# Kernel tuning notes

Measured on AMD Instinct MI355X. Metric: run time of the kernel, lower is better.

The kernel has to match this reference:

```python
import jax, jax.numpy as jnp
import numpy as np

N, E, G = 50000, 800000, 512
IN_C, H, EC, L, OUT_C = 16, 128, 16, 4, 1

def _lin(k, fi, fo):
    return jax.random.normal(k, (fi, fo), dtype=jnp.float32) / np.sqrt(fi)

def setup_inputs() -> dict:
    key = jax.random.key(0)
    ks = jax.random.split(key, 32)
    inp = {
        'x_nodes': jax.random.normal(ks[0], (N, IN_C), dtype=jnp.float32),
        'x_edges': jax.random.normal(ks[1], (E, EC), dtype=jnp.float32),
        'edge_index': jax.random.randint(ks[2], (2, E), 0, N),
        'batch': jnp.sort(jax.random.randint(ks[3], (N,), 0, G)),
    }
    # embed_nodes
    inp['emb_w1'] = _lin(ks[4], IN_C, H); inp['emb_b1'] = jnp.zeros((H,), jnp.float32)
    inp['emb_w2'] = _lin(ks[5], H, H);    inp['emb_b2'] = jnp.zeros((H,), jnp.float32)
    # per-layer edge_net / node_net weights, stacked over L
    kk = jax.random.split(ks[6], 4 * L)
    inp['ew1'] = jnp.stack([_lin(kk[i], 2 * H + EC, H) for i in range(L)])
    inp['eb1'] = jnp.zeros((L, H), jnp.float32)
    inp['ew2'] = jnp.stack([_lin(kk[L + i], H, H) for i in range(L)])
    inp['eb2'] = jnp.zeros((L, H), jnp.float32)
    inp['nw1'] = jnp.stack([_lin(kk[2 * L + i], 2 * H, H) for i in range(L)])
    inp['nb1'] = jnp.zeros((L, H), jnp.float32)
    inp['nw2'] = jnp.stack([_lin(kk[3 * L + i], H, H) for i in range(L)])
    inp['nb2'] = jnp.zeros((L, H), jnp.float32)
    # pre_readout / readout
    inp['pr_w1'] = _lin(ks[7], H, H); inp['pr_b1'] = jnp.zeros((H,), jnp.float32)
    inp['pr_w2'] = _lin(ks[8], H, H); inp['pr_b2'] = jnp.zeros((H,), jnp.float32)
    inp['ro_w1'] = _lin(ks[9], H, H); inp['ro_b1'] = jnp.zeros((H,), jnp.float32)
    inp['ro_w2'] = _lin(ks[10], H, OUT_C); inp['ro_b2'] = jnp.zeros((OUT_C,), jnp.float32)
    return inp

def _gnn_forward(x_nodes, x_edges, emb_w1, emb_b1, emb_w2, emb_b2,
                 ew1, eb1, ew2, eb2, nw1, nb1, nw2, nb2,
                 pr_w1, pr_b1, pr_w2, pr_b2, ro_w1, ro_b1, ro_w2, ro_b2,
                 edge_index, batch):
    silu = jax.nn.silu
    sender, receiver = edge_index[0], edge_index[1]
    # embed_nodes
    h = silu(x_nodes @ emb_w1 + emb_b1) @ emb_w2 + emb_b2  # [N, H]
    for l in range(L):
        state = jnp.concatenate((h[sender], h[receiver], x_edges), axis=1)  # [E, 2H+EC]
        msg = silu(silu(state @ ew1[l] + eb1[l]) @ ew2[l] + eb2[l])  # [E, H]
        aggr = jax.ops.segment_sum(msg, receiver, num_segments=N)  # [N, H]
        h = silu(jnp.concatenate((h, aggr), axis=1) @ nw1[l] + nb1[l]) @ nw2[l] + nb2[l]
    h = silu(h @ pr_w1 + pr_b1) @ pr_w2 + pr_b2
    pooled = jax.ops.segment_sum(h, batch, num_segments=G)  # [G, H]
    out = silu(pooled @ ro_w1 + ro_b1) @ ro_w2 + ro_b2  # [G, 1]
    return jnp.squeeze(out)

def reference(x_nodes, x_edges, edge_index, batch,
              emb_w1, emb_b1, emb_w2, emb_b2,
              ew1, eb1, ew2, eb2, nw1, nb1, nw2, nb2,
              pr_w1, pr_b1, pr_w2, pr_b2, ro_w1, ro_b1, ro_w2, ro_b2):
    return _gnn_forward(x_nodes, x_edges, emb_w1, emb_b1, emb_w2, emb_b2,
                        ew1, eb1, ew2, eb2, nw1, nb1, nw2, nb2,
                        pr_w1, pr_b1, pr_w2, pr_b2, ro_w1, ro_b1, ro_w2, ro_b2,
                        edge_index, batch)
```

## Files before the change

### kernel.cpp

```cpp
#include <hip/hip_runtime.h>


typedef short bf16x8 __attribute__((ext_vector_type(8)));
typedef float f32x4 __attribute__((ext_vector_type(4)));

union U8 { bf16x8 v; unsigned short u[8]; unsigned int d[4]; };

__device__ __forceinline__ float bf2f(unsigned short u) {
    union { unsigned int i; float f; } x; x.i = ((unsigned int)u) << 16; return x.f;
}
__device__ __forceinline__ float u32lo2f(unsigned int d) {
    union { unsigned int i; float f; } x; x.i = d << 16; return x.f;
}
__device__ __forceinline__ float u32hi2f(unsigned int d) {
    union { unsigned int i; float f; } x; x.i = d & 0xffff0000u; return x.f;
}
__device__ __forceinline__ unsigned short f2bf(float f) {
    union { float f; unsigned int i; } x; x.f = f;
    unsigned int r = x.i + 0x7FFFu + ((x.i >> 16) & 1u);
    return (unsigned short)(r >> 16);
}
__device__ __forceinline__ unsigned int cvt_pk_bf16(float lo, float hi) {
    unsigned int r;
    asm("v_cvt_pk_bf16_f32 %0, %1, %2" : "=v"(r) : "v"(lo), "v"(hi));
    return r;
}
__device__ __forceinline__ float siluf(float x) { return x / (1.0f + __expf(-x)); }
__device__ __forceinline__ float silu_fast(float x) {
    float e;
    asm("v_exp_f32 %0, %1" : "=v"(e) : "v"(x * -1.44269504089f));
    float r;
    asm("v_rcp_f32 %0, %1" : "=v"(r) : "v"(e + 1.0f));
    return x * r;
}

__global__ void k_hist(const int* __restrict__ recv, int* __restrict__ counts, int E) {
    int i = blockIdx.x * 256 + threadIdx.x;
    if (i < E) atomicAdd(&counts[recv[i]], 1);
}

__global__ __launch_bounds__(1024) void k_scan1(const int* __restrict__ counts,
                                                int* __restrict__ offsets,
                                                int* __restrict__ bsum, int n) {
    __shared__ int buf[1024];
    int i = blockIdx.x * 1024 + threadIdx.x;
    int v = (i < n) ? counts[i] : 0;
    buf[threadIdx.x] = v;
    __syncthreads();
    for (int off = 1; off < 1024; off <<= 1) {
        int t = 0;
        if ((int)threadIdx.x >= off) t = buf[threadIdx.x - off];
        __syncthreads();
        if ((int)threadIdx.x >= off) buf[threadIdx.x] += t;
        __syncthreads();
    }
    if (i < n) offsets[i] = buf[threadIdx.x] - v;
    if (threadIdx.x == 1023) bsum[blockIdx.x] = buf[1023];
}

__global__ void k_scan2(int* __restrict__ bsum, int nb) {
    if (threadIdx.x == 0 && blockIdx.x == 0) {
        int acc = 0;
        for (int b = 0; b < nb; ++b) { int v = bsum[b]; bsum[b] = acc; acc += v; }
    }
}

__global__ __launch_bounds__(1024) void k_scan3(int* __restrict__ offsets,
                                                const int* __restrict__ bsum,
                                                int n, int E) {
    int i = blockIdx.x * 1024 + threadIdx.x;
    if (i < n) offsets[i] += bsum[blockIdx.x];
    if (i == 0) offsets[n] = E;
}

__global__ void k_scatter(const int* __restrict__ send, const int* __restrict__ recv,
                          const int* __restrict__ offsets, int* __restrict__ cursor,
                          int* __restrict__ ss, int* __restrict__ sr,
                          int* __restrict__ perm, int E) {
    int i = blockIdx.x * 256 + threadIdx.x;
    if (i < E) {
        int r = recv[i];
        int pos = offsets[r] + atomicAdd(&cursor[r], 1);
        ss[pos] = send[i];
        sr[pos] = r;
        perm[pos] = i;
    }
}

__global__ void k_permute_xe(const float* __restrict__ xe, const int* __restrict__ perm,
                             unsigned short* __restrict__ out, int E) {
    int t = blockIdx.x * 256 + threadIdx.x;
    if (t < E * 4) {
        int pos = t >> 2, q = t & 3;
        int e = perm[pos];
        float4 v = *(const float4*)(xe + (size_t)e * 16 + q * 4);
        ushort4 o;
        o.x = f2bf(v.x); o.y = f2bf(v.y); o.z = f2bf(v.z); o.w = f2bf(v.w);
        *(ushort4*)(out + (size_t)pos * 16 + q * 4) = o;
    }
}

struct WJob { const float* src; unsigned short* dst; int rows; int perm; };
struct WJobs { WJob j[31]; };

__global__ __launch_bounds__(256) void k_wconv(WJobs jobs) {
    WJob jb = jobs.j[blockIdx.x];
    int n = jb.rows * 128;
    if (jb.perm) {
        for (int i = threadIdx.x; i < n; i += 256) {
            int c = i >> 7, slot = i & 127;
            int feat = (slot >> 3) + 16 * (slot & 7);
            jb.dst[c * 128 + slot] = f2bf(jb.src[feat * 128 + c]);
        }
    } else {
        for (int i = threadIdx.x; i < n; i += 256) {
            int k = i >> 7, c = i & 127;
            jb.dst[c * jb.rows + k] = f2bf(jb.src[i]);
        }
    }
}

__global__ __launch_bounds__(256) void k_embed1(const float* __restrict__ x,
                                                const float* __restrict__ w1,
                                                const float* __restrict__ b1,
                                                unsigned short* __restrict__ out, int N) {
    int idx = blockIdx.x * 256 + threadIdx.x;
    int n = idx >> 6, lane = idx & 63;
    if (n >= N) return;
    const float* xr = x + (size_t)n * 16;
    float xv[16];
#pragma unroll
    for (int k = 0; k < 16; k += 4) {
        float4 v = *(const float4*)(xr + k);
        xv[k] = v.x; xv[k + 1] = v.y; xv[k + 2] = v.z; xv[k + 3] = v.w;
    }
    int c0 = lane * 2;
    float a0 = b1[c0], a1 = b1[c0 + 1];
#pragma unroll
    for (int k = 0; k < 16; ++k) {
        float2 w = *(const float2*)(w1 + k * 128 + c0);
        a0 += xv[k] * w.x; a1 += xv[k] * w.y;
    }
    *(unsigned int*)(out + (size_t)n * 128 + c0) = cvt_pk_bf16(siluf(a0), siluf(a1));
}

__device__ __forceinline__ void load_frags(const unsigned short* __restrict__ A,
                                           int r0, int colb, int kg, int M,
                                           bf16x8 (&Af)[2][4]) {
#pragma unroll
    for (int rf = 0; rf < 2; ++rf) {
        int row = r0 + rf * 16 + colb;
        if (row < M) {
#pragma unroll
            for (int ks = 0; ks < 4; ++ks)
                Af[rf][ks] = *(const bf16x8*)(A + (size_t)row * 128 + ks * 32 + kg * 8);
        } else {
            U8 z;
#pragma unroll
            for (int i = 0; i < 8; ++i) z.u[i] = 0;
#pragma unroll
            for (int ks = 0; ks < 4; ++ks) Af[rf][ks] = z.v;
        }
    }
}

__device__ __forceinline__ void mma_block(const bf16x8 (&Af)[2][4],
                                          const unsigned short* sW,
                                          int colb, int kg, f32x4 (&C)[2][8]) {
#pragma unroll
    for (int ks = 0; ks < 4; ++ks) {
#pragma unroll
        for (int cf = 0; cf < 8; ++cf) {
            bf16x8 B = *(const bf16x8*)(sW + (colb + 16 * cf) * 136 + ks * 32 + kg * 8);
#pragma unroll
            for (int rf = 0; rf < 2; ++rf)
                C[rf][cf] = __builtin_amdgcn_mfma_f32_16x16x32_bf16(Af[rf][ks], B, C[rf][cf], 0, 0, 0);
        }
    }
}

#define WLOAD(WT) do { \
    _Pragma("unroll") \
    for (int k_ = 0; k_ < 8; ++k_) \
        wreg[k_] = *(const bf16x8*)((WT) + tid * 8 + k_ * 2048); \
} while (0)

#define WWRITE() do { __syncthreads(); \
    _Pragma("unroll") \
    for (int k_ = 0; k_ < 8; ++k_) { \
        int i_ = tid * 8 + k_ * 2048; \
        *(bf16x8*)(sW + (i_ >> 7) * 136 + (i_ & 127)) = wreg[k_]; \
    } \
    __syncthreads(); } while (0)

__global__ __launch_bounds__(256, 2) void k_node(
    const unsigned short* __restrict__ A1, const unsigned short* __restrict__ WT1,
    const unsigned short* __restrict__ A2, const unsigned short* __restrict__ WT2,
    const float* __restrict__ b12, int act1,
    unsigned short* __restrict__ out1,
    const unsigned short* __restrict__ WT3, const float* __restrict__ b3,
    unsigned short* __restrict__ out3,
    const unsigned short* __restrict__ WTs, const unsigned short* __restrict__ WTr,
    unsigned short* __restrict__ outPs, unsigned short* __restrict__ outPr,
    int M) {
    __shared__ unsigned short sW[128 * 136];
    __shared__ unsigned short sT[128 * 136];
    int tid = threadIdx.x, lane = tid & 63, w = tid >> 6;
    int r0 = blockIdx.x * 128 + w * 32;
    int colb = lane & 15, kg = lane >> 4;
    bf16x8 wreg[8];

    f32x4 C[2][8];
#pragma unroll
    for (int cf = 0; cf < 8; ++cf) {
        float bb = b12[colb + 16 * cf];
        C[0][cf] = (f32x4){bb, bb, bb, bb};
        C[1][cf] = C[0][cf];
    }
    bf16x8 Af[2][4], Af2[2][4];
    WLOAD(WT1);
    load_frags(A1, r0, colb, kg, M, Af);
    if (WT2) load_frags(A2, r0, colb, kg, M, Af2);
    WWRITE();
    if (WT2) WLOAD(WT2);
    mma_block(Af, sW, colb, kg, C);
    if (WT2) {
        WWRITE();
        if (WT3) WLOAD(WT3);
        mma_block(Af2, sW, colb, kg, C);
    } else if (WT3) {
        WLOAD(WT3);
    }
#pragma unroll
    for (int rf = 0; rf < 2; ++rf) {
#pragma unroll
        for (int cf = 0; cf < 8; ++cf) {
            int col = colb + 16 * cf;
#pragma unroll
            for (int j = 0; j < 4; ++j) {
                float v = C[rf][cf][j];
                if (act1) v = siluf(v);
                unsigned short bv = f2bf(v);
                int lrow = w * 32 + rf * 16 + kg * 4 + j;
                sT[lrow * 136 + col] = bv;
                if (out1) {
                    int row = r0 + rf * 16 + kg * 4 + j;
                    if (row < M) out1[(size_t)row * 128 + col] = bv;
                }
            }
        }
    }

    if (WT3) {
        WWRITE();
        if (WTs) WLOAD(WTs);
        bf16x8 At[2][4];
#pragma unroll
        for (int rf = 0; rf < 2; ++rf)
#pragma unroll
            for (int ks = 0; ks < 4; ++ks)
                At[rf][ks] = *(const bf16x8*)(sT + (w * 32 + rf * 16 + colb) * 136 + ks * 32 + kg * 8);
#pragma unroll
        for (int cf = 0; cf < 8; ++cf) {
            float bb = b3[colb + 16 * cf];
            C[0][cf] = (f32x4){bb, bb, bb, bb};
            C[1][cf] = C[0][cf];
        }
        mma_block(At, sW, colb, kg, C);
#pragma unroll
        for (int rf = 0; rf < 2; ++rf) {
#pragma unroll
            for (int cf = 0; cf < 8; ++cf) {
                int col = colb + 16 * cf;
#pragma unroll
                for (int j = 0; j < 4; ++j) {
                    unsigned short bv = f2bf(C[rf][cf][j]);
                    int row = r0 + rf * 16 + kg * 4 + j;
                    if (row < M) out3[(size_t)row * 128 + col] = bv;
                    if (WTs) sT[(w * 32 + rf * 16 + kg * 4 + j) * 136 + col] = bv;
                }
            }
        }
    } else if (WTs) {
        WLOAD(WTs);
    }

    if (WTs) {
        WWRITE();
        WLOAD(WTr);
        bf16x8 At[2][4];
#pragma unroll
        for (int rf = 0; rf < 2; ++rf)
#pragma unroll
            for (int ks = 0; ks < 4; ++ks)
                At[rf][ks] = *(const bf16x8*)(sT + (w * 32 + rf * 16 + colb) * 136 + ks * 32 + kg * 8);
#pragma unroll
        for (int rf = 0; rf < 2; ++rf)
#pragma unroll
            for (int cf = 0; cf < 8; ++cf) C[rf][cf] = (f32x4){0.f, 0.f, 0.f, 0.f};
        mma_block(At, sW, colb, kg, C);
#pragma unroll
        for (int rf = 0; rf < 2; ++rf) {
#pragma unroll
            for (int j = 0; j < 4; ++j) {
                int row = r0 + rf * 16 + kg * 4 + j;
                if (row < M) {
                    U8 o;
#pragma unroll
                    for (int q = 0; q < 4; ++q)
                        o.d[q] = cvt_pk_bf16(C[rf][2 * q][j], C[rf][2 * q + 1][j]);
                    *(bf16x8*)(outPs + (size_t)row * 128 + colb * 8) = o.v;
                }
            }
        }
        WWRITE();
#pragma unroll
        for (int rf = 0; rf < 2; ++rf)
#pragma unroll
            for (int cf = 0; cf < 8; ++cf) C[rf][cf] = (f32x4){0.f, 0.f, 0.f, 0.f};
        mma_block(At, sW, colb, kg, C);
#pragma unroll
        for (int rf = 0; rf < 2; ++rf) {
#pragma unroll
            for (int j = 0; j < 4; ++j) {
                int row = r0 + rf * 16 + kg * 4 + j;
                if (row < M) {
                    U8 o;
#pragma unroll
                    for (int q = 0; q < 4; ++q)
                        o.d[q] = cvt_pk_bf16(C[rf][2 * q][j], C[rf][2 * q + 1][j]);
                    *(bf16x8*)(outPr + (size_t)row * 128 + colb * 8) = o.v;
                }
            }
        }
    }
}

__global__ __launch_bounds__(256, 3) void k_msg(
    const unsigned short* __restrict__ Ps, const unsigned short* __restrict__ Pr,
    const unsigned short* __restrict__ xes,
    const int* __restrict__ ss, const int* __restrict__ sr,
    const unsigned short* __restrict__ WeT, const float* __restrict__ b1,
    const unsigned short* __restrict__ W2T, const float* __restrict__ b2,
    unsigned short* __restrict__ aggr, float* __restrict__ pbuf,
    int* __restrict__ pid, int ntiles) {
    __shared__ unsigned short sW2[128 * 136];
    __shared__ unsigned short sT[64 * 136];
    __shared__ float sB2[128];
    __shared__ int sRid[64];
    int tid = threadIdx.x, lane = tid & 63, w = tid >> 6;
    int colb = lane & 15, kg = lane >> 4;
    int R0 = w * 16, rb = R0 + kg * 4;

    for (int i = tid * 8; i < 16384; i += 2048)
        *(bf16x8*)(sW2 + (i >> 7) * 136 + (i & 127)) = *(const bf16x8*)(W2T + i);
    if (tid < 128) sB2[tid] = b2[tid];
    bf16x8 WeB[8];
#pragma unroll
    for (int cf = 0; cf < 8; ++cf) {
        if (kg < 2) WeB[cf] = *(const bf16x8*)(WeT + (colb + 16 * cf) * 16 + kg * 8);
        else { U8 z; for (int i = 0; i < 8; ++i) z.u[i] = 0; WeB[cf] = z.v; }
    }
    float b1v[8];
#pragma unroll
    for (int cf = 0; cf < 8; ++cf) b1v[cf] = b1[colb + 16 * cf];
    int s = lane * 2;
    int c0 = (s >> 3) + 16 * (s & 7);
    __syncthreads();

    int stride = gridDim.x;
    int t = blockIdx.x;
    U8 zz; for (int i = 0; i < 8; ++i) zz.u[i] = 0;
    bf16x8 Axe = zz.v;
    U8 gp[8];
    int4 s4 = *(const int4*)(ss + (t << 6) + rb);
    int4 r4 = *(const int4*)(sr + (t << 6) + rb);

#define ISSUE_GATHER(S4, R4, TT) do { \
        gp[0].v = *(const bf16x8*)(Ps + (size_t)(S4).x * 128 + colb * 8); \
        gp[1].v = *(const bf16x8*)(Ps + (size_t)(S4).y * 128 + colb * 8); \
        gp[2].v = *(const bf16x8*)(Ps + (size_t)(S4).z * 128 + colb * 8); \
        gp[3].v = *(const bf16x8*)(Ps + (size_t)(S4).w * 128 + colb * 8); \
        gp[4].v = *(const bf16x8*)(Pr + (size_t)(R4).x * 128 + colb * 8); \
        gp[5].v = *(const bf16x8*)(Pr + (size_t)(R4).y * 128 + colb * 8); \
        gp[6].v = *(const bf16x8*)(Pr + (size_t)(R4).z * 128 + colb * 8); \
        gp[7].v = *(const bf16x8*)(Pr + (size_t)(R4).w * 128 + colb * 8); \
        if (kg < 2) Axe = *(const bf16x8*)(xes + (size_t)(((TT) << 6) + R0 + colb) * 16 + kg * 8); \
    } while (0)

    ISSUE_GATHER(s4, r4, t);
    for (;;) {
        if (colb == 0) {
            sRid[rb] = r4.x; sRid[rb + 1] = r4.y; sRid[rb + 2] = r4.z; sRid[rb + 3] = r4.w;
        }
        int tn = t + stride;
        bool more = tn < ntiles;
        int4 s4n, r4n;
        if (more) {
            s4n = *(const int4*)(ss + (tn << 6) + rb);
            r4n = *(const int4*)(sr + (tn << 6) + rb);
        }
        f32x4 xc[8];
#pragma unroll
        for (int cf = 0; cf < 8; ++cf) {
            f32x4 bb = (f32x4){b1v[cf], b1v[cf], b1v[cf], b1v[cf]};
            xc[cf] = __builtin_amdgcn_mfma_f32_16x16x32_bf16(Axe, WeB[cf], bb, 0, 0, 0);
        }
#pragma unroll
        for (int j = 0; j < 4; ++j) {
            U8 o;
#pragma unroll
            for (int q = 0; q < 4; ++q) {
                float v0 = u32lo2f(gp[j].d[q]) + u32lo2f(gp[4 + j].d[q]) + xc[2 * q][j];
                float v1 = u32hi2f(gp[j].d[q]) + u32hi2f(gp[4 + j].d[q]) + xc[2 * q + 1][j];
                o.d[q] = cvt_pk_bf16(silu_fast(v0), silu_fast(v1));
            }
            *(bf16x8*)(sT + (rb + j) * 136 + colb * 8) = o.v;
        }
        int tcur = t;
        if (more) ISSUE_GATHER(s4n, r4n, tn);
        asm volatile("s_waitcnt lgkmcnt(0)" ::: "memory");
        __builtin_amdgcn_sched_barrier(0);
        bf16x8 Bt[4];
#pragma unroll
        for (int ks = 0; ks < 4; ++ks)
            Bt[ks] = *(const bf16x8*)(sT + (R0 + colb) * 136 + ks * 32 + kg * 8);
        f32x4 m[8];
#pragma unroll
        for (int acf = 0; acf < 8; ++acf)
            m[acf] = *(const f32x4*)(sB2 + acf * 16 + kg * 4);
#pragma unroll
        for (int ks = 0; ks < 4; ++ks) {
#pragma unroll
            for (int acf = 0; acf < 8; ++acf) {
                bf16x8 Aw = *(const bf16x8*)(sW2 + (16 * acf + colb) * 136 + ks * 32 + kg * 8);
                m[acf] = __builtin_amdgcn_mfma_f32_16x16x32_bf16(Aw, Bt[ks], m[acf], 0, 0, 0);
            }
        }
#pragma unroll
        for (int j = 0; j < 4; ++j) {
            U8 o;
#pragma unroll
            for (int q = 0; q < 4; ++q)
                o.d[q] = cvt_pk_bf16(silu_fast(m[2 * q][j]), silu_fast(m[2 * q + 1][j]));
            *(bf16x8*)(sT + (R0 + colb) * 136 + (kg * 4 + j) * 8) = o.v;
        }
        asm volatile("s_waitcnt lgkmcnt(0)" ::: "memory");
        __builtin_amdgcn_sched_barrier(0);
        {
            int run = tcur * 4 + w;
            float a0 = 0.f, a1 = 0.f;
            int prev = sRid[R0];
            bool first = true;
            for (int i = 0; i < 16; ++i) {
                int rid = sRid[R0 + i];
                if (rid != prev) {
                    if (first) {
                        float2 vv; vv.x = a0; vv.y = a1;
                        *(float2*)(pbuf + (size_t)(2 * run) * 128 + s) = vv;
                        if (lane == 0) pid[2 * run] = prev;
                        first = false;
                    } else {
                        aggr[(size_t)prev * 128 + c0] = f2bf(a0);
                        aggr[(size_t)prev * 128 + c0 + 16] = f2bf(a1);
                    }
                    a0 = 0.f; a1 = 0.f; prev = rid;
                }
                unsigned int v = *(const unsigned int*)(sT + (R0 + i) * 136 + s);
                a0 += u32lo2f(v); a1 += u32hi2f(v);
            }
            float2 vv; vv.x = a0; vv.y = a1;
            if (first) {
                *(float2*)(pbuf + (size_t)(2 * run) * 128 + s) = vv;
                if (lane == 0) { pid[2 * run] = prev; pid[2 * run + 1] = -1; }
            } else {
                *(float2*)(pbuf + (size_t)(2 * run + 1) * 128 + s) = vv;
                if (lane == 0) pid[2 * run + 1] = prev;
            }
        }
        if (!more) break;
        s4 = s4n; r4 = r4n; t = tn;
    }
#undef ISSUE_GATHER
}

__global__ __launch_bounds__(256) void k_fix(
    const float* __restrict__ pbuf, const int* __restrict__ pid,
    const int* __restrict__ offsets, unsigned short* __restrict__ aggr, int N) {
    int gw = (blockIdx.x * 256 + threadIdx.x) >> 6;
    int lane = threadIdx.x & 63;
    int nw = (gridDim.x * 256) >> 6;
    int s = lane * 2;
    int c0 = (s >> 3) + 16 * (s & 7);
    for (int n = gw; n < N; n += nw) {
        int o0 = offsets[n], o1 = offsets[n + 1];
        if (o0 >= o1) continue;
        int t0 = o0 >> 4, t1 = (o1 - 1) >> 4;
        if (t0 == t1 && o0 > (t0 << 4) && o1 <= (t0 << 4) + 15) continue;
        float a0 = 0.f, a1 = 0.f;
        for (int tt = t0; tt <= t1; ++tt) {
            if (pid[2 * tt] == n) {
                float2 v = *(const float2*)(pbuf + (size_t)(2 * tt) * 128 + s);
                a0 += v.x; a1 += v.y;
            }
            if (pid[2 * tt + 1] == n) {
                float2 v = *(const float2*)(pbuf + (size_t)(2 * tt + 1) * 128 + s);
                a0 += v.x; a1 += v.y;
            }
        }
        aggr[(size_t)n * 128 + c0] = f2bf(a0);
        aggr[(size_t)n * 128 + c0 + 16] = f2bf(a1);
    }
}

__device__ __forceinline__ int lowerb(const int* a, int n, int v) {
    int lo = 0, hi = n;
    while (lo < hi) { int mid = (lo + hi) >> 1; if (a[mid] < v) lo = mid + 1; else hi = mid; }
    return lo;
}

__global__ __launch_bounds__(128) void k_pool(const unsigned short* __restrict__ hpr,
                                              const int* __restrict__ batch,
                                              float* __restrict__ pooled, int N) {
    __shared__ int s_lo, s_hi;
    int g = blockIdx.x;
    if (threadIdx.x == 0) { s_lo = lowerb(batch, N, g); s_hi = lowerb(batch, N, g + 1); }
    __syncthreads();
    int c = threadIdx.x;
    float acc = 0.f;
    for (int r = s_lo; r < s_hi; ++r) acc += bf2f(hpr[(size_t)r * 128 + c]);
    pooled[(size_t)g * 128 + c] = acc;
}

__global__ __launch_bounds__(128) void k_readout(const float* __restrict__ pooled,
                                                 const float* __restrict__ w1,
                                                 const float* __restrict__ b1,
                                                 const float* __restrict__ w2,
                                                 const float* __restrict__ b2,
                                                 float* __restrict__ out) {
    __shared__ float sp[128];
    __shared__ float sred[2];
    int g = blockIdx.x, t = threadIdx.x;
    sp[t] = pooled[(size_t)g * 128 + t];
    __syncthreads();
    float acc = b1[t];
    for (int k = 0; k < 128; ++k) acc += sp[k] * w1[k * 128 + t];
    float val = siluf(acc) * w2[t];
#pragma unroll
    for (int off = 32; off; off >>= 1) val += __shfl_down(val, off);
    if ((t & 63) == 0) sred[t >> 6] = val;
    __syncthreads();
    if (t == 0) out[g] = sred[0] + sred[1] + b2[0];
}

extern "C" void kernel_launch(void* const* d_in, const int* in_sizes, int n_in,
                              void* d_out, int out_size, void* d_ws, size_t ws_size,
                              hipStream_t stream) {
    const float* x_nodes = (const float*)d_in[0];
    const float* x_edges = (const float*)d_in[1];
    const int* edge_index = (const int*)d_in[2];
    const int* batch = (const int*)d_in[3];
    const float* emb_w1 = (const float*)d_in[4];
    const float* emb_b1 = (const float*)d_in[5];
    const float* emb_w2 = (const float*)d_in[6];
    const float* emb_b2 = (const float*)d_in[7];
    const float* ew1 = (const float*)d_in[8];
    const float* eb1 = (const float*)d_in[9];
    const float* ew2 = (const float*)d_in[10];
    const float* eb2 = (const float*)d_in[11];
    const float* nw1 = (const float*)d_in[12];
    const float* nb1 = (const float*)d_in[13];
    const float* nw2 = (const float*)d_in[14];
    const float* nb2 = (const float*)d_in[15];
    const float* pr_w1 = (const float*)d_in[16];
    const float* pr_b1 = (const float*)d_in[17];
    const float* pr_w2 = (const float*)d_in[18];
    const float* pr_b2 = (const float*)d_in[19];
    const float* ro_w1 = (const float*)d_in[20];
    const float* ro_b1 = (const float*)d_in[21];
    const float* ro_w2 = (const float*)d_in[22];
    const float* ro_b2 = (const float*)d_in[23];

    const int N = in_sizes[0] / 16;
    const int E = in_sizes[1] / 16;
    const int G = 512;
    const int L = 4;
    const int nruns = E >> 4;
    const int ntiles = E >> 6;

    char* p = (char*)d_ws;
    auto alloc = [&](size_t bytes) {
        void* r = p;
        p += (bytes + 255) & ~(size_t)255;
        return r;
    };
    int* counts = (int*)alloc((size_t)N * 4);
    int* cursor = (int*)alloc((size_t)N * 4);
    int* offsets = (int*)alloc((size_t)(N + 1) * 4);
    int* bsum = (int*)alloc((size_t)256 * 4);
    int* ss = (int*)alloc((size_t)E * 4);
    int* sr = (int*)alloc((size_t)E * 4);
    int* perm = (int*)alloc((size_t)E * 4);
    unsigned short* xes = (unsigned short*)alloc((size_t)E * 16 * 2);
    unsigned short* h = (unsigned short*)alloc((size_t)N * 128 * 2);
    unsigned short* t0buf = (unsigned short*)alloc((size_t)N * 128 * 2);
    unsigned short* Ps = (unsigned short*)alloc((size_t)N * 128 * 2);
    unsigned short* Pr = (unsigned short*)alloc((size_t)N * 128 * 2);
    unsigned short* aggr = (unsigned short*)alloc((size_t)N * 128 * 2);
    unsigned short* hpr = (unsigned short*)alloc((size_t)N * 128 * 2);
    float* pooled = (float*)alloc((size_t)G * 128 * 4);
    float* pbuf = (float*)alloc((size_t)nruns * 2 * 128 * 4);
    int* pid = (int*)alloc((size_t)nruns * 2 * 4);

    const size_t WSZ = 128 * 128;
    unsigned short* wt_emb2 = (unsigned short*)alloc(WSZ * 2);
    unsigned short *wtWs[4], *wtWr[4], *wtWe[4], *wtW2[4], *wtN1a[4], *wtN1b[4], *wtN2[4];
    for (int l = 0; l < L; ++l) {
        wtWs[l] = (unsigned short*)alloc(WSZ * 2);
        wtWr[l] = (unsigned short*)alloc(WSZ * 2);
        wtWe[l] = (unsigned short*)alloc((size_t)16 * 128 * 2);
        wtW2[l] = (unsigned short*)alloc(WSZ * 2);
        wtN1a[l] = (unsigned short*)alloc(WSZ * 2);
        wtN1b[l] = (unsigned short*)alloc(WSZ * 2);
        wtN2[l] = (unsigned short*)alloc(WSZ * 2);
    }
    unsigned short* wt_pr1 = (unsigned short*)alloc(WSZ * 2);
    unsigned short* wt_pr2 = (unsigned short*)alloc(WSZ * 2);

    const int* send = edge_index;
    const int* recv = edge_index + E;

    hipMemsetAsync(counts, 0, (size_t)N * 4, stream);
    hipMemsetAsync(cursor, 0, (size_t)N * 4, stream);
    hipMemsetAsync(aggr, 0, (size_t)N * 128 * 2, stream);
    k_hist<<<(E + 255) / 256, 256, 0, stream>>>(recv, counts, E);
    int nb = (N + 1023) / 1024;
    k_scan1<<<nb, 1024, 0, stream>>>(counts, offsets, bsum, N);
    k_scan2<<<1, 64, 0, stream>>>(bsum, nb);
    k_scan3<<<nb, 1024, 0, stream>>>(offsets, bsum, N, E);
    k_scatter<<<(E + 255) / 256, 256, 0, stream>>>(send, recv, offsets, cursor, ss, sr, perm, E);
    k_permute_xe<<<(E * 4 + 255) / 256, 256, 0, stream>>>(x_edges, perm, xes, E);

    WJobs jobs;
    int nj = 0;
    auto addj = [&](const float* s, unsigned short* d, int rows, int pm) {
        jobs.j[nj].src = s; jobs.j[nj].dst = d; jobs.j[nj].rows = rows; jobs.j[nj].perm = pm; ++nj;
    };
    addj(emb_w2, wt_emb2, 128, 0);
    for (int l = 0; l < L; ++l) {
        const float* ew1_l = ew1 + (size_t)l * 272 * 128;
        addj(ew1_l, wtWs[l], 128, 0);
        addj(ew1_l + 128 * 128, wtWr[l], 128, 0);
        addj(ew1_l + 256 * 128, wtWe[l], 16, 0);
        addj(ew2 + (size_t)l * WSZ, wtW2[l], 128, 1);
        const float* nw1_l = nw1 + (size_t)l * 256 * 128;
        addj(nw1_l, wtN1a[l], 128, 0);
        addj(nw1_l + 128 * 128, wtN1b[l], 128, 0);
        addj(nw2 + (size_t)l * WSZ, wtN2[l], 128, 0);
    }
    addj(pr_w1, wt_pr1, 128, 0);
    addj(pr_w2, wt_pr2, 128, 0);
    k_wconv<<<nj, 256, 0, stream>>>(jobs);

    int gb = (N + 127) / 128;
    k_embed1<<<(N * 64 + 255) / 256, 256, 0, stream>>>(x_nodes, emb_w1, emb_b1, t0buf, N);
    k_node<<<gb, 256, 0, stream>>>(t0buf, wt_emb2, nullptr, nullptr, emb_b2, 0,
                                   h, nullptr, nullptr, nullptr,
                                   wtWs[0], wtWr[0], Ps, Pr, N);

    int mg = ntiles < 2048 ? ntiles : 2048;
    for (int l = 0; l < L; ++l) {
        k_msg<<<mg, 256, 0, stream>>>(Ps, Pr, xes, ss, sr, wtWe[l], eb1 + l * 128,
                                      wtW2[l], eb2 + l * 128, aggr, pbuf, pid, ntiles);
        k_fix<<<1024, 256, 0, stream>>>(pbuf, pid, offsets, aggr, N);
        k_node<<<gb, 256, 0, stream>>>(h, wtN1a[l], aggr, wtN1b[l], nb1 + l * 128, 1,
                                       nullptr, wtN2[l], nb2 + l * 128, h,
                                       (l < L - 1) ? wtWs[l + 1] : nullptr,
                                       (l < L - 1) ? wtWr[l + 1] : nullptr,
                                       Ps, Pr, N);
    }

    k_node<<<gb, 256, 0, stream>>>(h, wt_pr1, nullptr, nullptr, pr_b1, 1,
                                   nullptr, wt_pr2, pr_b2, hpr,
                                   nullptr, nullptr, nullptr, nullptr, N);
    k_pool<<<G, 128, 0, stream>>>(hpr, batch, pooled, N);
    k_readout<<<G, 128, 0, stream>>>(pooled, ro_w1, ro_b1, ro_w2, ro_b2, (float*)d_out);
}
```

Baseline: 921.8 us.

## Deepen edge-message gather pipeline to two tiles ahead with double-buffered registers

The message kernel now keeps two sets of gather registers (gpA/gpB and AxeA/AxeB) and prefetches neighbor-row gathers two tiles ahead, with index loads three tiles ahead. The loop is unrolled by two so the buffers alternate, giving more time to hide the latency of the random global gathers. This raises per-thread register use, which may lower occupancy. Separately, the fix-up kernel's grid is doubled from 1024 to 2048 blocks.

Measured after the change: 1.279 ms. 1.39x slower.

```diff
diff --git a/kernel.cpp b/kernel.cpp
--- a/kernel.cpp
+++ b/kernel.cpp
@@ -371,117 +371,162 @@
     int stride = gridDim.x;
     int t = blockIdx.x;
     U8 zz; for (int i = 0; i < 8; ++i) zz.u[i] = 0;
-    bf16x8 Axe = zz.v;
-    U8 gp[8];
-    int4 s4 = *(const int4*)(ss + (t << 6) + rb);
-    int4 r4 = *(const int4*)(sr + (t << 6) + rb);
-
-#define ISSUE_GATHER(S4, R4, TT) do { \
-        gp[0].v = *(const bf16x8*)(Ps + (size_t)(S4).x * 128 + colb * 8); \
-        gp[1].v = *(const bf16x8*)(Ps + (size_t)(S4).y * 128 + colb * 8); \
-        gp[2].v = *(const bf16x8*)(Ps + (size_t)(S4).z * 128 + colb * 8); \
-        gp[3].v = *(const bf16x8*)(Ps + (size_t)(S4).w * 128 + colb * 8); \
-        gp[4].v = *(const bf16x8*)(Pr + (size_t)(R4).x * 128 + colb * 8); \
-        gp[5].v = *(const bf16x8*)(Pr + (size_t)(R4).y * 128 + colb * 8); \
-        gp[6].v = *(const bf16x8*)(Pr + (size_t)(R4).z * 128 + colb * 8); \
-        gp[7].v = *(const bf16x8*)(Pr + (size_t)(R4).w * 128 + colb * 8); \
-        if (kg < 2) Axe = *(const bf16x8*)(xes + (size_t)(((TT) << 6) + R0 + colb) * 16 + kg * 8); \
-    } while (0)
-
-    ISSUE_GATHER(s4, r4, t);
+    bf16x8 AxeA = zz.v, AxeB = zz.v;
+    U8 gpA[8], gpB[8];
+
+    bool m1 = (t + stride) < ntiles;
+    bool m2 = (t + 2 * stride) < ntiles;
+    bool m3;
+    int4 s40 = *(const int4*)(ss + (t << 6) + rb);
+    int4 r40 = *(const int4*)(sr + (t << 6) + rb);
+    int4 r4cur = r40, r4nxt, s4pre, r4pre, s4new, r4new;
+    if (m1) {
+        int tn = t + stride;
+        int4 s41 = *(const int4*)(ss + (tn << 6) + rb);
+        r4nxt = *(const int4*)(sr + (tn << 6) + rb);
+        gpB[0].v = *(const bf16x8*)(Ps + (size_t)s41.x * 128 + colb * 8);
+        gpB[1].v = *(const bf16x8*)(Ps + (size_t)s41.y * 128 + colb * 8);
+        gpB[2].v = *(const bf16x8*)(Ps + (size_t)s41.z * 128 + colb * 8);
+        gpB[3].v = *(const bf16x8*)(Ps + (size_t)s41.w * 128 + colb * 8);
+        gpB[4].v = *(const bf16x8*)(Pr + (size_t)r4nxt.x * 128 + colb * 8);
+        gpB[5].v = *(const bf16x8*)(Pr + (size_t)r4nxt.y * 128 + colb * 8);
+        gpB[6].v = *(const bf16x8*)(Pr + (size_t)r4nxt.z * 128 + colb * 8);
+        gpB[7].v = *(const bf16x8*)(Pr + (size_t)r4nxt.w * 128 + colb * 8);
+        if (kg < 2) AxeB = *(const bf16x8*)(xes + (size_t)((tn << 6) + R0 + colb) * 16 + kg * 8);
+    }
+    if (m2) {
+        int t2 = t + 2 * stride;
+        s4pre = *(const int4*)(ss + (t2 << 6) + rb);
+        r4pre = *(const int4*)(sr + (t2 << 6) + rb);
+    }
+    gpA[0].v = *(const bf16x8*)(Ps + (size_t)s40.x * 128 + colb * 8);
+    gpA[1].v = *(const bf16x8*)(Ps + (size_t)s40.y * 128 + colb * 8);
+    gpA[2].v = *(const bf16x8*)(Ps + (size_t)s40.z * 128 + colb * 8);
+    gpA[3].v = *(const bf16x8*)(Ps + (size_t)s40.w * 128 + colb * 8);
+    gpA[4].v = *(const bf16x8*)(Pr + (size_t)r40.x * 128 + colb * 8);
+    gpA[5].v = *(const bf16x8*)(Pr + (size_t)r40.y * 128 + colb * 8);
+    gpA[6].v = *(const bf16x8*)(Pr + (size_t)r40.z * 128 + colb * 8);
+    gpA[7].v = *(const bf16x8*)(Pr + (size_t)r40.w * 128 + colb * 8);
+    if (kg < 2) AxeA = *(const bf16x8*)(xes + (size_t)((t << 6) + R0 + colb) * 16 + kg * 8);
+
+#define MSG_BODY(GP, AXE) do { \
+    if (colb == 0) { \
+        sRid[rb] = r4cur.x; sRid[rb + 1] = r4cur.y; \
+        sRid[rb + 2] = r4cur.z; sRid[rb + 3] = r4cur.w; \
+    } \
+    m3 = (t + 3 * stride) < ntiles; \
+    if (m3) { \
+        int t3_ = t + 3 * stride; \
+        s4new = *(const int4*)(ss + (t3_ << 6) + rb); \
+        r4new = *(const int4*)(sr + (t3_ << 6) + rb); \
+    } \
+    f32x4 xc[8]; \
+    _Pragma("unroll") \
+    for (int cf = 0; cf < 8; ++cf) { \
+        f32x4 bb = (f32x4){b1v[cf], b1v[cf], b1v[cf], b1v[cf]}; \
+        xc[cf] = __builtin_amdgcn_mfma_f32_16x16x32_bf16(AXE, WeB[cf], bb, 0, 0, 0); \
+    } \
+    _Pragma("unroll") \
+    for (int j = 0; j < 4; ++j) { \
+        U8 o; \
+        _Pragma("unroll") \
+        for (int q = 0; q < 4; ++q) { \
+            float v0 = u32lo2f(GP[j].d[q]) + u32lo2f(GP[4 + j].d[q]) + xc[2 * q][j]; \
+            float v1 = u32hi2f(GP[j].d[q]) + u32hi2f(GP[4 + j].d[q]) + xc[2 * q + 1][j]; \
+            o.d[q] = cvt_pk_bf16(silu_fast(v0), silu_fast(v1)); \
+        } \
+        *(bf16x8*)(sT + (rb + j) * 136 + colb * 8) = o.v; \
+    } \
+    if (m2) { \
+        int t2_ = t + 2 * stride; \
+        GP[0].v = *(const bf16x8*)(Ps + (size_t)s4pre.x * 128 + colb * 8); \
+        GP[1].v = *(const bf16x8*)(Ps + (size_t)s4pre.y * 128 + colb * 8); \
+        GP[2].v = *(const bf16x8*)(Ps + (size_t)s4pre.z * 128 + colb * 8); \
+        GP[3].v = *(const bf16x8*)(Ps + (size_t)s4pre.w * 128 + colb * 8); \
+        GP[4].v = *(const bf16x8*)(Pr + (size_t)r4pre.x * 128 + colb * 8); \
+        GP[5].v = *(const bf16x8*)(Pr + (size_t)r4pre.y * 128 + colb * 8); \
+        GP[6].v = *(const bf16x8*)(Pr + (size_t)r4pre.z * 128 + colb * 8); \
+        GP[7].v = *(const bf16x8*)(Pr + (size_t)r4pre.w * 128 + colb * 8); \
+        if (kg < 2) AXE = *(const bf16x8*)(xes + (size_t)((t2_ << 6) + R0 + colb) * 16 + kg * 8); \
+    } \
+    asm volatile("s_waitcnt lgkmcnt(0)" ::: "memory"); \
+    __builtin_amdgcn_sched_barrier(0); \
+    bf16x8 Bt[4]; \
+    _Pragma("unroll") \
+    for (int ks = 0; ks < 4; ++ks) \
+        Bt[ks] = *(const bf16x8*)(sT + (R0 + colb) * 136 + ks * 32 + kg * 8); \
+    f32x4 m[8]; \
+    _Pragma("unroll") \
+    for (int acf = 0; acf < 8; ++acf) \
+        m[acf] = *(const f32x4*)(sB2 + acf * 16 + kg * 4); \
+    _Pragma("unroll") \
+    for (int ks = 0; ks < 4; ++ks) { \
+        _Pragma("unroll") \
+        for (int acf = 0; acf < 8; ++acf) { \
+            bf16x8 Aw = *(const bf16x8*)(sW2 + (16 * acf + colb) * 136 + ks * 32 + kg * 8); \
+            m[acf] = __builtin_amdgcn_mfma_f32_16x16x32_bf16(Aw, Bt[ks], m[acf], 0, 0, 0); \
+        } \
+    } \
+    _Pragma("unroll") \
+    for (int j = 0; j < 4; ++j) { \
+        U8 o; \
+        _Pragma("unroll") \
+        for (int q = 0; q < 4; ++q) \
+            o.d[q] = cvt_pk_bf16(silu_fast(m[2 * q][j]), silu_fast(m[2 * q + 1][j])); \
+        *(bf16x8*)(sT + (R0 + colb) * 136 + (kg * 4 + j) * 8) = o.v; \
+    } \
+    asm volatile("s_waitcnt lgkmcnt(0)" ::: "memory"); \
+    __builtin_amdgcn_sched_barrier(0); \
+    { \
+        int run = t * 4 + w; \
+        float a0 = 0.f, a1 = 0.f; \
+        int prev = sRid[R0]; \
+        bool first = true; \
+        for (int i = 0; i < 16; ++i) { \
+            int rid = sRid[R0 + i]; \
+            if (rid != prev) { \
+                if (first) { \
+                    float2 vv; vv.x = a0; vv.y = a1; \
+                    *(float2*)(pbuf + (size_t)(2 * run) * 128 + s) = vv; \
+                    if (lane == 0) pid[2 * run] = prev; \
+                    first = false; \
+                } else { \
+                    aggr[(size_t)prev * 128 + c0] = f2bf(a0); \
+                    aggr[(size_t)prev * 128 + c0 + 16] = f2bf(a1); \
+                } \
+                a0 = 0.f; a1 = 0.f; prev = rid; \
+            } \
+            unsigned int v = *(const unsigned int*)(sT + (R0 + i) * 136 + s); \
+            a0 += u32lo2f(v); a1 += u32hi2f(v); \
+        } \
+        float2 vv; vv.x = a0; vv.y = a1; \
+        if (first) { \
+            *(float2*)(pbuf + (size_t)(2 * run) * 128 + s) = vv; \
+            if (lane == 0) { pid[2 * run] = prev; pid[2 * run + 1] = -1; } \
+        } else { \
+            *(float2*)(pbuf + (size_t)(2 * run + 1) * 128 + s) = vv; \
+            if (lane == 0) pid[2 * run + 1] = prev; \
+        } \
+    } \
+} while (0)
+
+#define MSG_ROTATE() do { \
+    t += stride; \
+    r4cur = r4nxt; r4nxt = r4pre; \
+    s4pre = s4new; r4pre = r4new; \
+    m1 = m2; m2 = m3; \
+} while (0)
+
     for (;;) {
-        if (colb == 0) {
-            sRid[rb] = r4.x; sRid[rb + 1] = r4.y; sRid[rb + 2] = r4.z; sRid[rb + 3] = r4.w;
-        }
-        int tn = t + stride;
-        bool more = tn < ntiles;
-        int4 s4n, r4n;
-        if (more) {
-            s4n = *(const int4*)(ss + (tn << 6) + rb);
-            r4n = *(const int4*)(sr + (tn << 6) + rb);
-        }
-        f32x4 xc[8];
-#pragma unroll
-        for (int cf = 0; cf < 8; ++cf) {
-            f32x4 bb = (f32x4){b1v[cf], b1v[cf], b1v[cf], b1v[cf]};
-            xc[cf] = __builtin_amdgcn_mfma_f32_16x16x32_bf16(Axe, WeB[cf], bb, 0, 0, 0);
-        }
-#pragma unroll
-        for (int j = 0; j < 4; ++j) {
-            U8 o;
-#pragma unroll
-            for (int q = 0; q < 4; ++q) {
-                float v0 = u32lo2f(gp[j].d[q]) + u32lo2f(gp[4 + j].d[q]) + xc[2 * q][j];
-                float v1 = u32hi2f(gp[j].d[q]) + u32hi2f(gp[4 + j].d[q]) + xc[2 * q + 1][j];
-                o.d[q] = cvt_pk_bf16(silu_fast(v0), silu_fast(v1));
-            }
-            *(bf16x8*)(sT + (rb + j) * 136 + colb * 8) = o.v;
-        }
-        int tcur = t;
-        if (more) ISSUE_GATHER(s4n, r4n, tn);
-        asm volatile("s_waitcnt lgkmcnt(0)" ::: "memory");
-        __builtin_amdgcn_sched_barrier(0);
-        bf16x8 Bt[4];
-#pragma unroll
-        for (int ks = 0; ks < 4; ++ks)
-            Bt[ks] = *(const bf16x8*)(sT + (R0 + colb) * 136 + ks * 32 + kg * 8);
-        f32x4 m[8];
-#pragma unroll
-        for (int acf = 0; acf < 8; ++acf)
-            m[acf] = *(const f32x4*)(sB2 + acf * 16 + kg * 4);
-#pragma unroll
-        for (int ks = 0; ks < 4; ++ks) {
-#pragma unroll
-            for (int acf = 0; acf < 8; ++acf) {
-                bf16x8 Aw = *(const bf16x8*)(sW2 + (16 * acf + colb) * 136 + ks * 32 + kg * 8);
-                m[acf] = __builtin_amdgcn_mfma_f32_16x16x32_bf16(Aw, Bt[ks], m[acf], 0, 0, 0);
-            }
-        }
-#pragma unroll
-        for (int j = 0; j < 4; ++j) {
-            U8 o;
-#pragma unroll
-            for (int q = 0; q < 4; ++q)
-                o.d[q] = cvt_pk_bf16(silu_fast(m[2 * q][j]), silu_fast(m[2 * q + 1][j]));
-            *(bf16x8*)(sT + (R0 + colb) * 136 + (kg * 4 + j) * 8) = o.v;
-        }
-        asm volatile("s_waitcnt lgkmcnt(0)" ::: "memory");
-        __builtin_amdgcn_sched_barrier(0);
-        {
-            int run = tcur * 4 + w;
-            float a0 = 0.f, a1 = 0.f;
-            int prev = sRid[R0];
-            bool first = true;
-            for (int i = 0; i < 16; ++i) {
-                int rid = sRid[R0 + i];
-                if (rid != prev) {
-                    if (first) {
-                        float2 vv; vv.x = a0; vv.y = a1;
-                        *(float2*)(pbuf + (size_t)(2 * run) * 128 + s) = vv;
-                        if (lane == 0) pid[2 * run] = prev;
-                        first = false;
-                    } else {
-                        aggr[(size_t)prev * 128 + c0] = f2bf(a0);
-                        aggr[(size_t)prev * 128 + c0 + 16] = f2bf(a1);
-                    }
-                    a0 = 0.f; a1 = 0.f; prev = rid;
-                }
-                unsigned int v = *(const unsigned int*)(sT + (R0 + i) * 136 + s);
-                a0 += u32lo2f(v); a1 += u32hi2f(v);
-            }
-            float2 vv; vv.x = a0; vv.y = a1;
-            if (first) {
-                *(float2*)(pbuf + (size_t)(2 * run) * 128 + s) = vv;
-                if (lane == 0) { pid[2 * run] = prev; pid[2 * run + 1] = -1; }
-            } else {
-                *(float2*)(pbuf + (size_t)(2 * run + 1) * 128 + s) = vv;
-                if (lane == 0) pid[2 * run + 1] = prev;
-            }
-        }
-        if (!more) break;
-        s4 = s4n; r4 = r4n; t = tn;
-    }
-#undef ISSUE_GATHER
+        MSG_BODY(gpA, AxeA);
+        if (!m1) break;
+        MSG_ROTATE();
+        MSG_BODY(gpB, AxeB);
+        if (!m1) break;
+        MSG_ROTATE();
+    }
+#undef MSG_BODY
+#undef MSG_ROTATE
 }
 
 __global__ __launch_bounds__(256) void k_fix(
@@ -672,7 +717,7 @@
     for (int l = 0; l < L; ++l) {
         k_msg<<<mg, 256, 0, stream>>>(Ps, Pr, xes, ss, sr, wtWe[l], eb1 + l * 128,
                                       wtW2[l], eb2 + l * 128, aggr, pbuf, pid, ntiles);
-        k_fix<<<1024, 256, 0, stream>>>(pbuf, pid, offsets, aggr, N);
+        k_fix<<<2048, 256, 0, stream>>>(pbuf, pid, offsets, aggr, N);
         k_node<<<gb, 256, 0, stream>>>(h, wtN1a[l], aggr, wtN1b[l], nb1 + l * 128, 1,
                                        nullptr, wtN2[l], nb2 + l * 128, h,
                                        (l < L - 1) ? wtWs[l + 1] : nullptr,
```
